# Kernel tuning notes

Measured on AMD Instinct MI355X. Metric: run time of the kernel, lower is better.

Reference implementation:

```python
import jax, jax.numpy as jnp
import numpy as np

HEADS = 8  # from init_kwargs

def setup_inputs() -> dict:
    key = jax.random.key(0)
    ks = jax.random.split(key, 7)
    B, C, H, W = 8, 256, 128, 128
    s = 1.0 / np.sqrt(C).astype(np.float32)
    return {
        "x": jax.random.normal(ks[0], (B, C, H, W), jnp.float32),
        "context": jax.random.normal(ks[1], (B, C, H, W), jnp.float32),
        "Wq": jax.random.normal(ks[2], (C, C), jnp.float32) * s,
        "Wkv": jax.random.normal(ks[3], (2 * C, C), jnp.float32) * s,
        "Wout": jax.random.normal(ks[4], (C, C), jnp.float32) * s,
        "Wscale": jax.random.normal(ks[5], (C, C), jnp.float32) * s,
        "Wshift": jax.random.normal(ks[6], (C, C), jnp.float32) * s,
    }

def reference(x, context, Wq, Wkv, Wout, Wscale, Wshift):
    B, C, H, W = x.shape
    h = HEADS
    e = C // h
    # mode='row': faithful raw reshape (NOT a permute), exactly as the torch code does
    xr = x.reshape(-1, W, C)        # [B*H, W, C] in raw row-major layout
    ctx = context.reshape(-1, W, C)
    q = xr @ Wq.T                   # nn.Linear: x @ W.T
    kv = xr @ Wkv.T
    k, v = kv[..., :C], kv[..., C:]
    scale = ctx @ Wscale.T
    shift = ctx @ Wshift.T
    # FiLM modulation on q, k, v
    q = scale * q + shift
    k = scale * k + shift
    v = scale * v + shift
    b = q.shape[0]
    split = lambda t: t.reshape(b, -1, h, e).transpose(0, 2, 1, 3)  # [b, h, t, e]
    qh, kh, vh = split(q), split(k), split(v)
    dots = jnp.einsum('bhie,bhje->bhij', qh, kh) * (e ** -0.5)
    attn = jax.nn.softmax(dots, axis=-1)
    out = jnp.einsum('bhij,bhje->bhie', attn, vh)    # [b, h, t, e]
    out = out.transpose(0, 2, 1, 3).reshape(b, -1, C)
    out = out @ Wout.T
    return out.reshape(B, C, H, W)
```

## Files before the change

### kernel.cpp

```cpp
#include <hip/hip_runtime.h>
#include <cstdint>

typedef short bf8 __attribute__((ext_vector_type(8)));
typedef float f4  __attribute__((ext_vector_type(4)));
typedef uint32_t u32x4 __attribute__((ext_vector_type(4)));
typedef unsigned short u16;

__device__ __forceinline__ u16 f2bf(float f) {
  union { float f; uint32_t u; } v; v.f = f;
  uint32_t u = v.u + 0x7fffu + ((v.u >> 16) & 1u);
  return (u16)(u >> 16);
}

__device__ __forceinline__ uint32_t pk2(float lo, float hi) {
  return (uint32_t)f2bf(lo) | ((uint32_t)f2bf(hi) << 16);
}

__device__ __forceinline__ bf8 ld_cvt8(const float* p) {
  f4 a = *(const f4*)p;
  f4 b = *(const f4*)(p + 4);
  u32x4 r;
  r[0] = pk2(a[0], a[1]);
  r[1] = pk2(a[2], a[3]);
  r[2] = pk2(b[0], b[1]);
  r[3] = pk2(b[2], b[3]);
  return __builtin_bit_cast(bf8, r);
}

template<bool WB>
__device__ __forceinline__ bf8 ldW(const void* p, size_t off) {
  if constexpr (WB) return *(const bf8*)((const u16*)p + off);
  else              return ld_cvt8((const float*)p + off);
}

#define MFMA(a, b, c) __builtin_amdgcn_mfma_f32_16x16x32_bf16((a), (b), (c), 0, 0, 0)

constexpr int SEQ = 128;
constexpr int CH  = 256;
constexpr int NH  = 8;

__global__ void cvt_weights(const float* __restrict__ wq, const float* __restrict__ wkv,
                            const float* __restrict__ wout, const float* __restrict__ wsc,
                            const float* __restrict__ wsh, u16* __restrict__ dst) {
  int i = (blockIdx.x * 256 + threadIdx.x) * 8;
  const float* s; int off;
  if      (i <  65536) { s = wq;   off = i; }
  else if (i < 196608) { s = wkv;  off = i -  65536; }
  else if (i < 262144) { s = wout; off = i - 196608; }
  else if (i < 327680) { s = wsc;  off = i - 262144; }
  else                 { s = wsh;  off = i - 327680; }
  *(bf8*)(dst + i) = ld_cvt8(s + off);
}

template<bool WB>
__global__ __launch_bounds__(256, 1)
void fused_axattn(const float* __restrict__ x,   const float* __restrict__ ctx,
                  const void* __restrict__ Wq,  const void* __restrict__ Wkv,
                  const void* __restrict__ Wout,const void* __restrict__ Wsc,
                  const void* __restrict__ Wsh, float* __restrict__ out)
{
  __shared__ u16 sQ[SEQ][40];
  __shared__ u16 sK[SEQ][40];
  __shared__ u16 sVT[32][136];
  __shared__ u16 sP[SEQ][136];
  __shared__ u16 sO[SEQ][264];

  const int tid  = threadIdx.x;
  const int wave = tid >> 6;
  const int lane = tid & 63;
  const int l15  = lane & 15;
  const int quad = lane >> 4;
  const int g    = blockIdx.x;
  const size_t gbase = (size_t)g * (SEQ * CH);
  const int ib = wave * 32;

  const float SCALE = 0.17677669529663687f;

  auto wrow = [&](const void* base, size_t row) -> const void* {
    if constexpr (WB) return (const void*)((const u16*)base + row * CH);
    else              return (const void*)((const float*)base + row * CH);
  };

  float rinv[2][4];

  for (int h = 0; h < NH; ++h) {
    f4 acc[2][10];
    #pragma unroll
    for (int mt = 0; mt < 2; ++mt)
      #pragma unroll
      for (int t = 0; t < 10; ++t) acc[mt][t] = 0.0f;

    const int hn0 = h * 32 + l15;
    const void* bp[10];
    bp[0] = wrow(Wq,  hn0);        bp[1] = wrow(Wq,  hn0 + 16);
    bp[2] = wrow(Wkv, hn0);        bp[3] = wrow(Wkv, hn0 + 16);
    bp[4] = wrow(Wkv, hn0 + 256);  bp[5] = wrow(Wkv, hn0 + 272);
    bp[6] = wrow(Wsc, hn0);        bp[7] = wrow(Wsc, hn0 + 16);
    bp[8] = wrow(Wsh, hn0);        bp[9] = wrow(Wsh, hn0 + 16);

    const float* axp = x   + gbase + (size_t)(ib + l15) * CH + quad * 8;
    const float* acp = ctx + gbase + (size_t)(ib + l15) * CH + quad * 8;

    #pragma unroll
    for (int kc = 0; kc < 8; ++kc) {
      const int cc = kc * 32;
      bf8 ax0 = ld_cvt8(axp + cc);
      bf8 ax1 = ld_cvt8(axp + 16 * CH + cc);
      bf8 ac0 = ld_cvt8(acp + cc);
      bf8 ac1 = ld_cvt8(acp + 16 * CH + cc);
      #pragma unroll
      for (int t = 0; t < 10; ++t) {
        bf8 b = ldW<WB>(bp[t], cc + quad * 8);
        bf8 a0 = (t < 6) ? ax0 : ac0;
        bf8 a1 = (t < 6) ? ax1 : ac1;
        acc[0][t] = MFMA(a0, b, acc[0][t]);
        acc[1][t] = MFMA(a1, b, acc[1][t]);
      }
    }

    #pragma unroll
    for (int mt = 0; mt < 2; ++mt) {
      #pragma unroll
      for (int r = 0; r < 4; ++r) {
        const int i = ib + 16 * mt + 4 * quad + r;
        const float sc0 = acc[mt][6][r], sc1 = acc[mt][7][r];
        const float sh0 = acc[mt][8][r], sh1 = acc[mt][9][r];
        sQ[i][l15]      = f2bf(sc0 * acc[mt][0][r] + sh0);
        sQ[i][16 + l15] = f2bf(sc1 * acc[mt][1][r] + sh1);
        sK[i][l15]      = f2bf(sc0 * acc[mt][2][r] + sh0);
        sK[i][16 + l15] = f2bf(sc1 * acc[mt][3][r] + sh1);
        sVT[l15][i]      = f2bf(sc0 * acc[mt][4][r] + sh0);
        sVT[16 + l15][i] = f2bf(sc1 * acc[mt][5][r] + sh1);
      }
    }
    __syncthreads();

    f4 sacc[2][8];
    #pragma unroll
    for (int mt = 0; mt < 2; ++mt) {
      const int i0 = ib + 16 * mt;
      bf8 a = *(const bf8*)(&sQ[i0 + l15][quad * 8]);
      #pragma unroll
      for (int ct = 0; ct < 8; ++ct) {
        bf8 b = *(const bf8*)(&sK[ct * 16 + l15][quad * 8]);
        f4 z = 0.0f;
        sacc[mt][ct] = MFMA(a, b, z);
      }
    }

    #pragma unroll
    for (int mt = 0; mt < 2; ++mt) {
      const int i0 = ib + 16 * mt;
      float mx[4] = {-3.4e38f, -3.4e38f, -3.4e38f, -3.4e38f};
      #pragma unroll
      for (int ct = 0; ct < 8; ++ct)
        #pragma unroll
        for (int r = 0; r < 4; ++r) mx[r] = fmaxf(mx[r], sacc[mt][ct][r]);
      #pragma unroll
      for (int m = 1; m <= 8; m <<= 1)
        #pragma unroll
        for (int r = 0; r < 4; ++r) mx[r] = fmaxf(mx[r], __shfl_xor(mx[r], m));

      float sm[4] = {0.f, 0.f, 0.f, 0.f};
      #pragma unroll
      for (int ct = 0; ct < 8; ++ct)
        #pragma unroll
        for (int r = 0; r < 4; ++r) {
          float p = __expf((sacc[mt][ct][r] - mx[r]) * SCALE);
          sm[r] += p;
          sP[i0 + 4 * quad + r][ct * 16 + l15] = f2bf(p);
        }
      #pragma unroll
      for (int m = 1; m <= 8; m <<= 1)
        #pragma unroll
        for (int r = 0; r < 4; ++r) sm[r] += __shfl_xor(sm[r], m);
      #pragma unroll
      for (int r = 0; r < 4; ++r) rinv[mt][r] = 1.0f / sm[r];
    }
    __syncthreads();

    #pragma unroll
    for (int mt = 0; mt < 2; ++mt) {
      const int i0 = ib + 16 * mt;
      #pragma unroll
      for (int dt = 0; dt < 2; ++dt) {
        f4 o = 0.0f;
        #pragma unroll
        for (int kt = 0; kt < 4; ++kt) {
          bf8 a = *(const bf8*)(&sP[i0 + l15][kt * 32 + quad * 8]);
          bf8 b = *(const bf8*)(&sVT[dt * 16 + l15][kt * 32 + quad * 8]);
          o = MFMA(a, b, o);
        }
        #pragma unroll
        for (int r = 0; r < 4; ++r)
          sO[i0 + 4 * quad + r][h * 32 + dt * 16 + l15] = f2bf(o[r] * rinv[mt][r]);
      }
    }
    __syncthreads();
  }

  f4 pacc[2][16];
  #pragma unroll
  for (int mt = 0; mt < 2; ++mt)
    #pragma unroll
    for (int nt = 0; nt < 16; ++nt) pacc[mt][nt] = 0.0f;

  #pragma unroll
  for (int kc = 0; kc < 8; ++kc) {
    const int cc = kc * 32;
    bf8 a0 = *(const bf8*)(&sO[ib + l15][cc + quad * 8]);
    bf8 a1 = *(const bf8*)(&sO[ib + 16 + l15][cc + quad * 8]);
    #pragma unroll
    for (int nt = 0; nt < 16; ++nt) {
      bf8 b = ldW<WB>(wrow(Wout, nt * 16 + l15), cc + quad * 8);
      pacc[0][nt] = MFMA(a0, b, pacc[0][nt]);
      pacc[1][nt] = MFMA(a1, b, pacc[1][nt]);
    }
  }

  #pragma unroll
  for (int mt = 0; mt < 2; ++mt)
    #pragma unroll
    for (int nt = 0; nt < 16; ++nt)
      #pragma unroll
      for (int r = 0; r < 4; ++r)
        out[gbase + (size_t)(ib + 16 * mt + 4 * quad + r) * CH + nt * 16 + l15] =
            pacc[mt][nt][r];
}

extern "C" void kernel_launch(void* const* d_in, const int* in_sizes, int n_in,
                              void* d_out, int out_size, void* d_ws, size_t ws_size,
                              hipStream_t stream) {
  const float* x    = (const float*)d_in[0];
  const float* ctx  = (const float*)d_in[1];
  const float* Wq   = (const float*)d_in[2];
  const float* Wkv  = (const float*)d_in[3];
  const float* Wout = (const float*)d_in[4];
  const float* Wsc  = (const float*)d_in[5];
  const float* Wsh  = (const float*)d_in[6];
  float* o = (float*)d_out;

  if (ws_size >= 393216u * sizeof(u16)) {
    u16* w = (u16*)d_ws;
    cvt_weights<<<dim3(192), dim3(256), 0, stream>>>(Wq, Wkv, Wout, Wsc, Wsh, w);
    fused_axattn<true><<<dim3(1024), dim3(256), 0, stream>>>(
        x, ctx, w, w + 65536, w + 196608, w + 262144, w + 327680, o);
  } else {
    fused_axattn<false><<<dim3(1024), dim3(256), 0, stream>>>(
        x, ctx, Wq, Wkv, Wout, Wsc, Wsh, o);
  }
}
```

Baseline: 1.015 ms.

## Pre-convert activations to bf16, fold output projection per head, raise occupancy

Result: slower. 1.279 ms (+26.0%).

```diff
diff --git a/kernel.cpp b/kernel.cpp
--- a/kernel.cpp
+++ b/kernel.cpp
@@ -33,11 +33,20 @@
   else              return ld_cvt8((const float*)p + off);
 }
 
+template<bool XB>
+__device__ __forceinline__ bf8 ldA(const float* xf, const u16* xb, size_t off) {
+  if constexpr (XB) return *(const bf8*)(xb + off);
+  else              return ld_cvt8(xf + off);
+}
+
 #define MFMA(a, b, c) __builtin_amdgcn_mfma_f32_16x16x32_bf16((a), (b), (c), 0, 0, 0)
 
 constexpr int SEQ = 128;
 constexpr int CH  = 256;
 constexpr int NH  = 8;
+
+constexpr size_t W_ELEMS = 393216;
+constexpr size_t X_ELEMS = 33554432ull;
 
 __global__ void cvt_weights(const float* __restrict__ wq, const float* __restrict__ wkv,
                             const float* __restrict__ wout, const float* __restrict__ wsc,
@@ -52,9 +61,30 @@
   *(bf8*)(dst + i) = ld_cvt8(s + off);
 }
 
-template<bool WB>
-__global__ __launch_bounds__(256, 1)
+__global__ void cvt_all(const float* __restrict__ wq, const float* __restrict__ wkv,
+                        const float* __restrict__ wout, const float* __restrict__ wsc,
+                        const float* __restrict__ wsh, const float* __restrict__ x,
+                        const float* __restrict__ ctx, u16* __restrict__ dst) {
+  const long nchunk = (long)((W_ELEMS + 2 * X_ELEMS) / 8);
+  for (long c = blockIdx.x * (long)blockDim.x + threadIdx.x; c < nchunk;
+       c += (long)gridDim.x * blockDim.x) {
+    long i = c * 8;
+    const float* s; long off;
+    if      (i <  65536)  { s = wq;   off = i; }
+    else if (i < 196608)  { s = wkv;  off = i -  65536; }
+    else if (i < 262144)  { s = wout; off = i - 196608; }
+    else if (i < 327680)  { s = wsc;  off = i - 262144; }
+    else if (i < 393216)  { s = wsh;  off = i - 327680; }
+    else if (i < (long)(W_ELEMS + X_ELEMS)) { s = x;   off = i - (long)W_ELEMS; }
+    else                                    { s = ctx; off = i - (long)(W_ELEMS + X_ELEMS); }
+    *(bf8*)(dst + i) = ld_cvt8(s + off);
+  }
+}
+
+template<bool WB, bool XB>
+__global__ __launch_bounds__(256, 2)
 void fused_axattn(const float* __restrict__ x,   const float* __restrict__ ctx,
+                  const u16* __restrict__ xb,    const u16* __restrict__ cb,
                   const void* __restrict__ Wq,  const void* __restrict__ Wkv,
                   const void* __restrict__ Wout,const void* __restrict__ Wsc,
                   const void* __restrict__ Wsh, float* __restrict__ out)
@@ -63,7 +93,7 @@
   __shared__ u16 sK[SEQ][40];
   __shared__ u16 sVT[32][136];
   __shared__ u16 sP[SEQ][136];
-  __shared__ u16 sO[SEQ][264];
+  __shared__ u16 sOh[SEQ][40];
 
   const int tid  = threadIdx.x;
   const int wave = tid >> 6;
@@ -82,14 +112,13 @@
   };
 
   float rinv[2][4];
+  f4 pacc[2][16];
+  #pragma unroll
+  for (int mt = 0; mt < 2; ++mt)
+    #pragma unroll
+    for (int nt = 0; nt < 16; ++nt) pacc[mt][nt] = 0.0f;
 
   for (int h = 0; h < NH; ++h) {
-    f4 acc[2][10];
-    #pragma unroll
-    for (int mt = 0; mt < 2; ++mt)
-      #pragma unroll
-      for (int t = 0; t < 10; ++t) acc[mt][t] = 0.0f;
-
     const int hn0 = h * 32 + l15;
     const void* bp[10];
     bp[0] = wrow(Wq,  hn0);        bp[1] = wrow(Wq,  hn0 + 16);
@@ -98,39 +127,36 @@
     bp[6] = wrow(Wsc, hn0);        bp[7] = wrow(Wsc, hn0 + 16);
     bp[8] = wrow(Wsh, hn0);        bp[9] = wrow(Wsh, hn0 + 16);
 
-    const float* axp = x   + gbase + (size_t)(ib + l15) * CH + quad * 8;
-    const float* acp = ctx + gbase + (size_t)(ib + l15) * CH + quad * 8;
-
-    #pragma unroll
-    for (int kc = 0; kc < 8; ++kc) {
-      const int cc = kc * 32;
-      bf8 ax0 = ld_cvt8(axp + cc);
-      bf8 ax1 = ld_cvt8(axp + 16 * CH + cc);
-      bf8 ac0 = ld_cvt8(acp + cc);
-      bf8 ac1 = ld_cvt8(acp + 16 * CH + cc);
-      #pragma unroll
-      for (int t = 0; t < 10; ++t) {
-        bf8 b = ldW<WB>(bp[t], cc + quad * 8);
-        bf8 a0 = (t < 6) ? ax0 : ac0;
-        bf8 a1 = (t < 6) ? ax1 : ac1;
-        acc[0][t] = MFMA(a0, b, acc[0][t]);
-        acc[1][t] = MFMA(a1, b, acc[1][t]);
-      }
-    }
-
-    #pragma unroll
-    for (int mt = 0; mt < 2; ++mt) {
+    #pragma unroll
+    for (int mt = 0; mt < 2; ++mt) {
+      f4 acc[10];
+      #pragma unroll
+      for (int t = 0; t < 10; ++t) acc[t] = 0.0f;
+
+      const size_t arow = gbase + (size_t)(ib + 16 * mt + l15) * CH;
+      #pragma unroll
+      for (int kc = 0; kc < 8; ++kc) {
+        const size_t cc = (size_t)kc * 32 + quad * 8;
+        bf8 ax = ldA<XB>(x,   xb, arow + cc);
+        bf8 ac = ldA<XB>(ctx, cb, arow + cc);
+        #pragma unroll
+        for (int t = 0; t < 10; ++t) {
+          bf8 b = ldW<WB>(bp[t], cc);
+          acc[t] = MFMA((t < 6) ? ax : ac, b, acc[t]);
+        }
+      }
+
       #pragma unroll
       for (int r = 0; r < 4; ++r) {
         const int i = ib + 16 * mt + 4 * quad + r;
-        const float sc0 = acc[mt][6][r], sc1 = acc[mt][7][r];
-        const float sh0 = acc[mt][8][r], sh1 = acc[mt][9][r];
-        sQ[i][l15]      = f2bf(sc0 * acc[mt][0][r] + sh0);
-        sQ[i][16 + l15] = f2bf(sc1 * acc[mt][1][r] + sh1);
-        sK[i][l15]      = f2bf(sc0 * acc[mt][2][r] + sh0);
-        sK[i][16 + l15] = f2bf(sc1 * acc[mt][3][r] + sh1);
-        sVT[l15][i]      = f2bf(sc0 * acc[mt][4][r] + sh0);
-        sVT[16 + l15][i] = f2bf(sc1 * acc[mt][5][r] + sh1);
+        const float sc0 = acc[6][r], sc1 = acc[7][r];
+        const float sh0 = acc[8][r], sh1 = acc[9][r];
+        sQ[i][l15]      = f2bf(sc0 * acc[0][r] + sh0);
+        sQ[i][16 + l15] = f2bf(sc1 * acc[1][r] + sh1);
+        sK[i][l15]      = f2bf(sc0 * acc[2][r] + sh0);
+        sK[i][16 + l15] = f2bf(sc1 * acc[3][r] + sh1);
+        sVT[l15][i]      = f2bf(sc0 * acc[4][r] + sh0);
+        sVT[16 + l15][i] = f2bf(sc1 * acc[5][r] + sh1);
       }
     }
     __syncthreads();
@@ -177,7 +203,7 @@
       #pragma unroll
       for (int r = 0; r < 4; ++r) rinv[mt][r] = 1.0f / sm[r];
     }
-    __syncthreads();
+    asm volatile("s_waitcnt lgkmcnt(0)" ::: "memory");
 
     #pragma unroll
     for (int mt = 0; mt < 2; ++mt) {
@@ -193,29 +219,22 @@
         }
         #pragma unroll
         for (int r = 0; r < 4; ++r)
-          sO[i0 + 4 * quad + r][h * 32 + dt * 16 + l15] = f2bf(o[r] * rinv[mt][r]);
+          sOh[i0 + 4 * quad + r][dt * 16 + l15] = f2bf(o[r] * rinv[mt][r]);
+      }
+    }
+    asm volatile("s_waitcnt lgkmcnt(0)" ::: "memory");
+
+    {
+      bf8 a0 = *(const bf8*)(&sOh[ib + l15][quad * 8]);
+      bf8 a1 = *(const bf8*)(&sOh[ib + 16 + l15][quad * 8]);
+      #pragma unroll
+      for (int nt = 0; nt < 16; ++nt) {
+        bf8 b = ldW<WB>(wrow(Wout, nt * 16 + l15), (size_t)h * 32 + quad * 8);
+        pacc[0][nt] = MFMA(a0, b, pacc[0][nt]);
+        pacc[1][nt] = MFMA(a1, b, pacc[1][nt]);
       }
     }
     __syncthreads();
-  }
-
-  f4 pacc[2][16];
-  #pragma unroll
-  for (int mt = 0; mt < 2; ++mt)
-    #pragma unroll
-    for (int nt = 0; nt < 16; ++nt) pacc[mt][nt] = 0.0f;
-
-  #pragma unroll
-  for (int kc = 0; kc < 8; ++kc) {
-    const int cc = kc * 32;
-    bf8 a0 = *(const bf8*)(&sO[ib + l15][cc + quad * 8]);
-    bf8 a1 = *(const bf8*)(&sO[ib + 16 + l15][cc + quad * 8]);
-    #pragma unroll
-    for (int nt = 0; nt < 16; ++nt) {
-      bf8 b = ldW<WB>(wrow(Wout, nt * 16 + l15), cc + quad * 8);
-      pacc[0][nt] = MFMA(a0, b, pacc[0][nt]);
-      pacc[1][nt] = MFMA(a1, b, pacc[1][nt]);
-    }
   }
 
   #pragma unroll
@@ -240,13 +259,22 @@
   const float* Wsh  = (const float*)d_in[6];
   float* o = (float*)d_out;
 
-  if (ws_size >= 393216u * sizeof(u16)) {
+  const size_t need_full = (W_ELEMS + 2 * X_ELEMS) * sizeof(u16);
+
+  if (ws_size >= need_full) {
+    u16* w  = (u16*)d_ws;
+    u16* xb = w + W_ELEMS;
+    u16* cb = xb + X_ELEMS;
+    cvt_all<<<dim3(8192), dim3(256), 0, stream>>>(Wq, Wkv, Wout, Wsc, Wsh, x, ctx, w);
+    fused_axattn<true, true><<<dim3(1024), dim3(256), 0, stream>>>(
+        x, ctx, xb, cb, w, w + 65536, w + 196608, w + 262144, w + 327680, o);
+  } else if (ws_size >= W_ELEMS * sizeof(u16)) {
     u16* w = (u16*)d_ws;
     cvt_weights<<<dim3(192), dim3(256), 0, stream>>>(Wq, Wkv, Wout, Wsc, Wsh, w);
-    fused_axattn<true><<<dim3(1024), dim3(256), 0, stream>>>(
-        x, ctx, w, w + 65536, w + 196608, w + 262144, w + 327680, o);
+    fused_axattn<true, false><<<dim3(1024), dim3(256), 0, stream>>>(
+        x, ctx, nullptr, nullptr, w, w + 65536, w + 196608, w + 262144, w + 327680, o);
   } else {
-    fused_axattn<false><<<dim3(1024), dim3(256), 0, stream>>>(
-        x, ctx, Wq, Wkv, Wout, Wsc, Wsh, o);
+    fused_axattn<false, false><<<dim3(1024), dim3(256), 0, stream>>>(
+        x, ctx, nullptr, nullptr, Wq, Wkv, Wout, Wsc, Wsh, o);
   }
 }
```
